# Optimization experiments

Hardware: AMD Instinct MI355X
Metric: run time of the kernel (lower is better)

The kernel has to match this reference:

```python
import jax, jax.numpy as jnp
import numpy as np

B, S, H = 2, 4096, 2048
NH, NKV, HD = 16, 4, 128          # heads, kv heads, head_dim = H // NH
GS_RATIO = 0.25                    # hardcoded in MyAttention.forward
ROPE_BASE = 10000.0


def rotate_half(x):
    h = x.shape[-1] // 2
    return jnp.concatenate((-x[..., h:], x[..., :h]), axis=-1)


def setup_inputs() -> dict:
    key = jax.random.key(0)
    ks = jax.random.split(key, 5)
    g = int(S * GS_RATIO)
    hidden_states = jax.random.normal(ks[0], (B, S, H), jnp.float32)
    position_ids = jnp.tile(jnp.arange(S, dtype=jnp.int32)[None, :], (B, 1))
    # causal additive mask per group window (0 keep, -1e9 masked)
    i = jnp.arange(g)
    causal = i[None, :] <= i[:, None]
    attention_mask = jnp.broadcast_to(
        jnp.where(causal, 0.0, -1e9).astype(jnp.float32)[None, None], (B, 1, g, g)
    )
    sc = 0.02
    Wq = (jax.random.normal(ks[1], (H, NH * HD), jnp.float32) * sc)
    Wk = (jax.random.normal(ks[2], (H, NKV * HD), jnp.float32) * sc)
    Wv = (jax.random.normal(ks[3], (H, NKV * HD), jnp.float32) * sc)
    Wo = (jax.random.normal(ks[4], (NH * HD, H), jnp.float32) * sc)
    return {"hidden_states": hidden_states, "attention_mask": attention_mask,
            "position_ids": position_ids, "Wq": Wq, "Wk": Wk, "Wv": Wv, "Wo": Wo}


def reference(hidden_states, attention_mask, position_ids, Wq, Wk, Wv, Wo):
    B_, S_, H_ = hidden_states.shape
    g = int(S_ * GS_RATIO)
    ng = S_ // g
    n_rep = NH // NKV

    # QKV projections -> (B, heads, S, HD)
    q = (hidden_states @ Wq).reshape(B_, S_, NH, HD).transpose(0, 2, 1, 3)
    k = (hidden_states @ Wk).reshape(B_, S_, NKV, HD).transpose(0, 2, 1, 3)
    v = (hidden_states @ Wv).reshape(B_, S_, NKV, HD).transpose(0, 2, 1, 3)

    # RoPE
    inv_freq = 1.0 / (ROPE_BASE ** (jnp.arange(0, HD, 2, dtype=jnp.float32) / HD))
    t = jnp.arange(S_, dtype=jnp.float32)
    emb = jnp.concatenate([jnp.outer(t, inv_freq)] * 2, axis=-1)  # (S, HD)
    cos = jnp.cos(emb)[position_ids][:, None]  # (B,1,S,HD)
    sin = jnp.sin(emb)[position_ids][:, None]
    q = q * cos + rotate_half(q) * sin
    k = k * cos + rotate_half(k) * sin

    # GQA repeat_kv
    k = jnp.repeat(k, n_rep, axis=1)
    v = jnp.repeat(v, n_rep, axis=1)

    # S2-Attn shift: roll second half of heads by -g/2 along seq, then group
    def shift(x):
        x = jnp.concatenate([x[:, :NH // 2],
                             jnp.roll(x[:, NH // 2:], -g // 2, axis=2)], axis=1)
        return x.transpose(0, 2, 1, 3).reshape(B_ * ng, g, NH, HD).transpose(0, 2, 1, 3)

    q, k, v = shift(q), shift(k), shift(v)

    attn = jnp.einsum('bhqd,bhkd->bhqk', q, k) / np.float32(np.sqrt(HD))
    mask = jnp.tile(attention_mask, (ng, 1, 1, 1))  # (B*ng,1,g,g)
    attn = attn + mask
    attn = jax.nn.softmax(attn.astype(jnp.float32), axis=-1).astype(q.dtype)

    out = jnp.einsum('bhqk,bhkd->bhqd', attn, v)  # (B*ng, NH, g, HD)
    out = out.transpose(0, 2, 1, 3).reshape(B_, S_, NH, HD)
    # undo shift for second half of heads (+g/2 along seq)
    out = jnp.concatenate([out[:, :, :NH // 2],
                           jnp.roll(out[:, :, NH // 2:], g // 2, axis=1)], axis=2)
    out = out.reshape(B_, S_, NH * HD) @ Wo
    return out
```

## Files before the change

### kernel.cpp

```cpp
#include <hip/hip_runtime.h>
#include <math.h>

typedef unsigned short u16;
typedef short bf16x8 __attribute__((ext_vector_type(8)));
typedef float f32x4 __attribute__((ext_vector_type(4)));


__device__ __forceinline__ u16 f2bf(float x) {
  union { float f; unsigned u; } c; c.f = x;
  unsigned r = (c.u + 0x7FFFu + ((c.u >> 16) & 1u)) >> 16;
  return (u16)r;
}
__device__ __forceinline__ float bf2f(u16 x) {
  union { unsigned u; float f; } c; c.u = ((unsigned)x) << 16;
  return c.f;
}

#define GLD16(gp, lp)                                                   \
  __builtin_amdgcn_global_load_lds(                                     \
      (__attribute__((address_space(1))) void*)(gp),                    \
      (__attribute__((address_space(3))) void*)(lp), 16, 0, 0)

__global__ __launch_bounds__(256) void cast_bf16_vec(
    const float* __restrict__ X, u16* __restrict__ Y) {
  const size_t i = ((size_t)blockIdx.x * 256 + threadIdx.x) * 4;
  float4 v = *(const float4*)(X + i);
  ushort4 o;
  o.x = f2bf(v.x); o.y = f2bf(v.y); o.z = f2bf(v.z); o.w = f2bf(v.w);
  *(ushort4*)(Y + i) = o;
}

__global__ __launch_bounds__(256) void wt_cast(
    const float* __restrict__ W, u16* __restrict__ Wt, int K, int N) {
  const int bk = blockIdx.y * 64;
  const int bn = blockIdx.x * 64;
  __shared__ float T[64 * 65];
  const int tid = threadIdx.x;
  #pragma unroll
  for (int u = 0; u < 16; ++u) {
    int idx = tid + u * 256;
    int kl = idx >> 6, nl = idx & 63;
    T[kl * 65 + nl] = W[(size_t)(bk + kl) * N + bn + nl];
  }
  __syncthreads();
  #pragma unroll
  for (int u = 0; u < 16; ++u) {
    int idx = tid + u * 256;
    int nl = idx >> 6, kl = idx & 63;
    Wt[(size_t)(bn + nl) * K + bk + kl] = f2bf(T[kl * 65 + nl]);
  }
}

__global__ __launch_bounds__(256) void gemm_bf16(
    const u16* __restrict__ A, const u16* __restrict__ Bt,
    float* __restrict__ Cf, u16* __restrict__ Cb, int M, int N, int K) {
  __shared__ u16 As[128 * 32];
  __shared__ u16 Bs[128 * 32];

  const int tid = threadIdx.x;
  const int bm = blockIdx.y * 128;
  const int bn = blockIdx.x * 128;
  const int w = tid >> 6, lane = tid & 63;
  const int col = lane & 15, quad = lane >> 4;
  const int mblk = (w & 1) * 64, nblk = (w >> 1) * 64;

  const int srow = tid >> 2;
  const int sseg = (tid & 3) * 8;

  const u16* ag0 = A + (size_t)(bm + srow) * K + sseg;
  const u16* ag1 = A + (size_t)(bm + 64 + srow) * K + sseg;
  const u16* bg0 = Bt + (size_t)(bn + srow) * K + sseg;
  const u16* bg1 = Bt + (size_t)(bn + 64 + srow) * K + sseg;
  u16* al = &As[srow * 32 + sseg];
  u16* bl = &Bs[srow * 32 + sseg];

  f32x4 acc[4][4];
  #pragma unroll
  for (int i = 0; i < 4; ++i)
    #pragma unroll
    for (int j = 0; j < 4; ++j) acc[i][j] = (f32x4)(0.0f);

  for (int k0 = 0; k0 < K; k0 += 32) {
    __syncthreads();
    GLD16(ag0 + k0, al);
    GLD16(ag1 + k0, al + 64 * 32);
    GLD16(bg0 + k0, bl);
    GLD16(bg1 + k0, bl + 64 * 32);
    __syncthreads();

    bf16x8 af[4], bfr[4];
    #pragma unroll
    for (int i = 0; i < 4; ++i)
      af[i] = *(const bf16x8*)&As[(mblk + 16 * i + col) * 32 + quad * 8];
    #pragma unroll
    for (int j = 0; j < 4; ++j)
      bfr[j] = *(const bf16x8*)&Bs[(nblk + 16 * j + col) * 32 + quad * 8];
    #pragma unroll
    for (int i = 0; i < 4; ++i)
      #pragma unroll
      for (int j = 0; j < 4; ++j)
        acc[i][j] = __builtin_amdgcn_mfma_f32_16x16x32_bf16(af[i], bfr[j], acc[i][j], 0, 0, 0);
  }

  #pragma unroll
  for (int i = 0; i < 4; ++i) {
    const int row0 = bm + mblk + 16 * i + quad * 4;
    #pragma unroll
    for (int j = 0; j < 4; ++j) {
      const int cc = bn + nblk + 16 * j + col;
      #pragma unroll
      for (int r = 0; r < 4; ++r) {
        if (Cb) Cb[(size_t)(row0 + r) * N + cc] = f2bf(acc[i][j][r]);
        else    Cf[(size_t)(row0 + r) * N + cc] = acc[i][j][r];
      }
    }
  }
}

__global__ __launch_bounds__(256) void rope_qkv(
    u16* __restrict__ QKV, const int* __restrict__ pos) {
  const unsigned idx = blockIdx.x * 256 + threadIdx.x;
  const int d = idx & 63;
  const unsigned rest = idx >> 6;
  const int hh = rest % 20;
  const unsigned bs = rest / 20;

  const int colbase = (hh < 16) ? hh * 128 : 2048 + (hh - 16) * 128;
  u16* p = QKV + (size_t)bs * 3072 + colbase + d;
  const float x0 = bf2f(p[0]);
  const float x1 = bf2f(p[64]);
  const float t = (float)pos[bs];
  const float inv_freq = __expf((float)d * -0.14391156509676332f);
  float s, c;
  __sincosf(t * inv_freq, &s, &c);
  const float sc = (hh < 16) ? 0.08838834764831845f : 1.0f;
  p[0]  = f2bf((x0 * c - x1 * s) * sc);
  p[64] = f2bf((x1 * c + x0 * s) * sc);
}

__global__ __launch_bounds__(256) void v_transpose(
    const u16* __restrict__ QKV, u16* __restrict__ Vt) {
  const int bid = blockIdx.x;
  const int st = bid & 63;
  const int kvh = (bid >> 6) & 3;
  const int b = bid >> 8;
  __shared__ u16 T[64 * 136];
  const int tid = threadIdx.x;
  #pragma unroll
  for (int u = 0; u < 4; ++u) {
    int idx = tid + u * 256;
    int sl = idx >> 4, ch = idx & 15;
    *(uint4*)&T[sl * 136 + ch * 8] =
        *(const uint4*)(QKV + ((size_t)(b * 4096 + st * 64 + sl)) * 3072 + 2560 + kvh * 128 + ch * 8);
  }
  __syncthreads();
  #pragma unroll
  for (int u = 0; u < 32; ++u) {
    int idx = tid + u * 256;
    int d = idx >> 6, sl = idx & 63;
    Vt[((size_t)((b * 4 + kvh) * 128 + d)) * 4096 + st * 64 + sl] = T[sl * 136 + d];
  }
}

__global__ __launch_bounds__(512, 4) void attn_mfma(
    const u16* __restrict__ QKV, const u16* __restrict__ Vt,
    u16* __restrict__ Ob) {
  __shared__ u16 Ks[64 * 136];
  __shared__ u16 Vs[128 * 72];
  __shared__ u16 Ps[8][16 * 72];

  const int bid = blockIdx.x;
  const int qt = 7 - (bid & 7);
  const int h  = (bid >> 3) & 15;
  const int gi = (bid >> 7) & 3;
  const int b  = bid >> 9;

  const int tid = threadIdx.x;
  const int w = tid >> 6, lane = tid & 63;
  const int col = lane & 15, quad = lane >> 4;

  const int shift = (h >= 8) ? 512 : 0;
  const int base_s = gi * 1024;
  const int kvh = h >> 2;
  const int ktmax = 2 * qt + 1;

  const int krow = tid >> 4, kch = tid & 15;
  const int vrow = tid >> 3, vch = tid & 7;

  const u16* ksrc = QKV + ((size_t)(b * 4096)) * 3072 + 2048 + kvh * 128;
  const u16* vsrc = Vt + ((size_t)((b * 4 + kvh) * 128)) * 4096;

  uint4 kreg[2], vreg[2];
  {
    const int sk0 = (base_s + shift) & 4095;
    kreg[0] = *(const uint4*)(ksrc + (size_t)(sk0 + krow) * 3072 + kch * 8);
    kreg[1] = *(const uint4*)(ksrc + (size_t)(sk0 + 32 + krow) * 3072 + kch * 8);
    vreg[0] = *(const uint4*)(vsrc + (size_t)vrow * 4096 + sk0 + vch * 8);
    vreg[1] = *(const uint4*)(vsrc + (size_t)(64 + vrow) * 4096 + sk0 + vch * 8);
  }

  bf16x8 aq[4];
  {
    const int qg = qt * 128 + w * 16 + col;
    const int sqr = (base_s + qg + shift) & 4095;
    const u16* qp = QKV + ((size_t)(b * 4096 + sqr)) * 3072 + h * 128;
    #pragma unroll
    for (int kk = 0; kk < 4; ++kk)
      aq[kk] = *(const bf16x8*)(qp + kk * 32 + quad * 8);
  }

  f32x4 o[8];
  #pragma unroll
  for (int jd = 0; jd < 8; ++jd) o[jd] = (f32x4)(0.0f);
  float lp[4] = {0.0f, 0.0f, 0.0f, 0.0f};

  u16* Pw = &Ps[w][0];
  const int qrow_l = qt * 128 + w * 16 + quad * 4;

  for (int kt = 0; kt <= ktmax; ++kt) {
    __syncthreads();
    *(uint4*)&Ks[krow * 136 + kch * 8] = kreg[0];
    *(uint4*)&Ks[(32 + krow) * 136 + kch * 8] = kreg[1];
    *(uint4*)&Vs[vrow * 72 + vch * 8] = vreg[0];
    *(uint4*)&Vs[(64 + vrow) * 72 + vch * 8] = vreg[1];
    __syncthreads();

    if (kt < ktmax) {
      const int skn = (base_s + (kt + 1) * 64 + shift) & 4095;
      kreg[0] = *(const uint4*)(ksrc + (size_t)(skn + krow) * 3072 + kch * 8);
      kreg[1] = *(const uint4*)(ksrc + (size_t)(skn + 32 + krow) * 3072 + kch * 8);
      vreg[0] = *(const uint4*)(vsrc + (size_t)vrow * 4096 + skn + vch * 8);
      vreg[1] = *(const uint4*)(vsrc + (size_t)(64 + vrow) * 4096 + skn + vch * 8);
    }

    f32x4 sc[4];
    #pragma unroll
    for (int j = 0; j < 4; ++j) sc[j] = (f32x4)(0.0f);
    #pragma unroll
    for (int kk = 0; kk < 4; ++kk) {
      #pragma unroll
      for (int j = 0; j < 4; ++j) {
        bf16x8 bk = *(const bf16x8*)&Ks[(16 * j + col) * 136 + kk * 32 + quad * 8];
        sc[j] = __builtin_amdgcn_mfma_f32_16x16x32_bf16(aq[kk], bk, sc[j], 0, 0, 0);
      }
    }

    if (kt >= 2 * qt) {
      #pragma unroll
      for (int j = 0; j < 4; ++j) {
        #pragma unroll
        for (int r = 0; r < 4; ++r) {
          float p = __expf(sc[j][r]);
          if ((kt * 64 + 16 * j + col) > (qrow_l + r)) p = 0.0f;
          lp[r] += p;
          Pw[(quad * 4 + r) * 72 + 16 * j + col] = f2bf(p);
        }
      }
    } else {
      #pragma unroll
      for (int j = 0; j < 4; ++j) {
        #pragma unroll
        for (int r = 0; r < 4; ++r) {
          float p = __expf(sc[j][r]);
          lp[r] += p;
          Pw[(quad * 4 + r) * 72 + 16 * j + col] = f2bf(p);
        }
      }
    }

    #pragma unroll
    for (int ks = 0; ks < 2; ++ks) {
      bf16x8 ap = *(const bf16x8*)&Pw[col * 72 + ks * 32 + quad * 8];
      #pragma unroll
      for (int jd = 0; jd < 8; ++jd) {
        bf16x8 bv = *(const bf16x8*)&Vs[(16 * jd + col) * 72 + ks * 32 + quad * 8];
        o[jd] = __builtin_amdgcn_mfma_f32_16x16x32_bf16(ap, bv, o[jd], 0, 0, 0);
      }
    }
  }

  #pragma unroll
  for (int r = 0; r < 4; ++r) {
    lp[r] += __shfl_xor(lp[r], 1, 64);
    lp[r] += __shfl_xor(lp[r], 2, 64);
    lp[r] += __shfl_xor(lp[r], 4, 64);
    lp[r] += __shfl_xor(lp[r], 8, 64);
  }

  #pragma unroll
  for (int r = 0; r < 4; ++r) {
    const int qg = qt * 128 + w * 16 + quad * 4 + r;
    const int sq = (base_s + qg + shift) & 4095;
    u16* dst = Ob + ((size_t)(b * 4096 + sq)) * 2048 + h * 128;
    const float inv = 1.0f / lp[r];
    #pragma unroll
    for (int jd = 0; jd < 8; ++jd)
      dst[16 * jd + col] = f2bf(o[jd][r] * inv);
  }
}

extern "C" void kernel_launch(void* const* d_in, const int* in_sizes, int n_in,
                              void* d_out, int out_size, void* d_ws, size_t ws_size,
                              hipStream_t stream) {
  const float* hs = (const float*)d_in[0];
  const int*   pos = (const int*)d_in[2];
  const float* Wq = (const float*)d_in[3];
  const float* Wk = (const float*)d_in[4];
  const float* Wv = (const float*)d_in[5];
  const float* Wo = (const float*)d_in[6];

  char* ws = (char*)d_ws;
  u16* hsb   = (u16*)ws; ws += (size_t)8192 * 2048 * 2;
  u16* Wqkvt = (u16*)ws; ws += (size_t)3072 * 2048 * 2;
  u16* Wot   = (u16*)ws; ws += (size_t)2048 * 2048 * 2;
  u16* QKVb  = (u16*)ws; ws += (size_t)8192 * 3072 * 2;
  u16* Vtt   = (u16*)ws; ws += (size_t)2 * 4 * 128 * 4096 * 2;
  u16* Obh   = (u16*)ws; ws += (size_t)8192 * 2048 * 2;

  dim3 blk(256);

  cast_bf16_vec<<<16384, blk, 0, stream>>>(hs, hsb);
  wt_cast<<<dim3(32, 32), blk, 0, stream>>>(Wq, Wqkvt, 2048, 2048);
  wt_cast<<<dim3(8, 32),  blk, 0, stream>>>(Wk, Wqkvt + (size_t)2048 * 2048, 2048, 512);
  wt_cast<<<dim3(8, 32),  blk, 0, stream>>>(Wv, Wqkvt + (size_t)2560 * 2048, 2048, 512);
  wt_cast<<<dim3(32, 32), blk, 0, stream>>>(Wo, Wot, 2048, 2048);

  gemm_bf16<<<dim3(24, 64), blk, 0, stream>>>(hsb, Wqkvt, nullptr, QKVb, 8192, 3072, 2048);

  rope_qkv<<<40960, blk, 0, stream>>>(QKVb, pos);
  v_transpose<<<512, blk, 0, stream>>>(QKVb, Vtt);

  attn_mfma<<<1024, dim3(512), 0, stream>>>(QKVb, Vtt, Obh);

  gemm_bf16<<<dim3(16, 64), blk, 0, stream>>>(Obh, Wot, (float*)d_out, nullptr, 8192, 2048, 2048);
}
```

Baseline: 606.6 us.

## Transpose score MFMA, vectorize P stores, drop K/V register prefetch for occupancy

Swaps the MFMA operand order so each lane holds four consecutive keys for one query, which lets P be written to LDS as packed ushort4 stores and reduces the row-sum to a single accumulator finished with two cross-lane shuffles. Removes the register double-buffered K/V prefetch and loads the current tile directly before the barrier, and raises the launch-bounds occupancy hint from 4 to 6. The aim is lower register pressure and fewer LDS store instructions, giving more resident waves per CU. In exchange, global load latency is no longer overlapped with compute inside a block and has to be hidden by the other resident waves.

```diff
diff --git a/kernel.cpp b/kernel.cpp
--- a/kernel.cpp
+++ b/kernel.cpp
@@ -162,7 +162,7 @@
   }
 }
 
-__global__ __launch_bounds__(512, 4) void attn_mfma(
+__global__ __launch_bounds__(512, 6) void attn_mfma(
     const u16* __restrict__ QKV, const u16* __restrict__ Vt,
     u16* __restrict__ Ob) {
   __shared__ u16 Ks[64 * 136];
@@ -190,15 +190,6 @@
   const u16* ksrc = QKV + ((size_t)(b * 4096)) * 3072 + 2048 + kvh * 128;
   const u16* vsrc = Vt + ((size_t)((b * 4 + kvh) * 128)) * 4096;
 
-  uint4 kreg[2], vreg[2];
-  {
-    const int sk0 = (base_s + shift) & 4095;
-    kreg[0] = *(const uint4*)(ksrc + (size_t)(sk0 + krow) * 3072 + kch * 8);
-    kreg[1] = *(const uint4*)(ksrc + (size_t)(sk0 + 32 + krow) * 3072 + kch * 8);
-    vreg[0] = *(const uint4*)(vsrc + (size_t)vrow * 4096 + sk0 + vch * 8);
-    vreg[1] = *(const uint4*)(vsrc + (size_t)(64 + vrow) * 4096 + sk0 + vch * 8);
-  }
-
   bf16x8 aq[4];
   {
     const int qg = qt * 128 + w * 16 + col;
@@ -212,59 +203,66 @@
   f32x4 o[8];
   #pragma unroll
   for (int jd = 0; jd < 8; ++jd) o[jd] = (f32x4)(0.0f);
-  float lp[4] = {0.0f, 0.0f, 0.0f, 0.0f};
+  float lsum = 0.0f;
 
   u16* Pw = &Ps[w][0];
-  const int qrow_l = qt * 128 + w * 16 + quad * 4;
+  const int qrow = qt * 128 + w * 16 + col;
 
   for (int kt = 0; kt <= ktmax; ++kt) {
+    const int sk0 = (base_s + kt * 64 + shift) & 4095;
+
+    uint4 k0 = *(const uint4*)(ksrc + (size_t)(sk0 + krow) * 3072 + kch * 8);
+    uint4 k1 = *(const uint4*)(ksrc + (size_t)(sk0 + 32 + krow) * 3072 + kch * 8);
+    uint4 v0 = *(const uint4*)(vsrc + (size_t)vrow * 4096 + sk0 + vch * 8);
+    uint4 v1 = *(const uint4*)(vsrc + (size_t)(64 + vrow) * 4096 + sk0 + vch * 8);
+
     __syncthreads();
-    *(uint4*)&Ks[krow * 136 + kch * 8] = kreg[0];
-    *(uint4*)&Ks[(32 + krow) * 136 + kch * 8] = kreg[1];
-    *(uint4*)&Vs[vrow * 72 + vch * 8] = vreg[0];
-    *(uint4*)&Vs[(64 + vrow) * 72 + vch * 8] = vreg[1];
+    *(uint4*)&Ks[krow * 136 + kch * 8] = k0;
+    *(uint4*)&Ks[(32 + krow) * 136 + kch * 8] = k1;
+    *(uint4*)&Vs[vrow * 72 + vch * 8] = v0;
+    *(uint4*)&Vs[(64 + vrow) * 72 + vch * 8] = v1;
     __syncthreads();
 
-    if (kt < ktmax) {
-      const int skn = (base_s + (kt + 1) * 64 + shift) & 4095;
-      kreg[0] = *(const uint4*)(ksrc + (size_t)(skn + krow) * 3072 + kch * 8);
-      kreg[1] = *(const uint4*)(ksrc + (size_t)(skn + 32 + krow) * 3072 + kch * 8);
-      vreg[0] = *(const uint4*)(vsrc + (size_t)vrow * 4096 + skn + vch * 8);
-      vreg[1] = *(const uint4*)(vsrc + (size_t)(64 + vrow) * 4096 + skn + vch * 8);
+    f32x4 sc[4];
+    #pragma unroll
+    for (int i = 0; i < 4; ++i) sc[i] = (f32x4)(0.0f);
+    #pragma unroll
+    for (int kk = 0; kk < 4; ++kk) {
+      #pragma unroll
+      for (int i = 0; i < 4; ++i) {
+        bf16x8 ak = *(const bf16x8*)&Ks[(16 * i + col) * 136 + kk * 32 + quad * 8];
+        sc[i] = __builtin_amdgcn_mfma_f32_16x16x32_bf16(ak, aq[kk], sc[i], 0, 0, 0);
+      }
     }
 
-    f32x4 sc[4];
-    #pragma unroll
-    for (int j = 0; j < 4; ++j) sc[j] = (f32x4)(0.0f);
-    #pragma unroll
-    for (int kk = 0; kk < 4; ++kk) {
-      #pragma unroll
-      for (int j = 0; j < 4; ++j) {
-        bf16x8 bk = *(const bf16x8*)&Ks[(16 * j + col) * 136 + kk * 32 + quad * 8];
-        sc[j] = __builtin_amdgcn_mfma_f32_16x16x32_bf16(aq[kk], bk, sc[j], 0, 0, 0);
-      }
-    }
-
-    if (kt >= 2 * qt) {
-      #pragma unroll
-      for (int j = 0; j < 4; ++j) {
-        #pragma unroll
-        for (int r = 0; r < 4; ++r) {
-          float p = __expf(sc[j][r]);
-          if ((kt * 64 + 16 * j + col) > (qrow_l + r)) p = 0.0f;
-          lp[r] += p;
-          Pw[(quad * 4 + r) * 72 + 16 * j + col] = f2bf(p);
-        }
+    if (kt * 64 + 63 > qt * 128 + w * 16) {
+      #pragma unroll
+      for (int i = 0; i < 4; ++i) {
+        ushort4 pk;
+        float p0 = __expf(sc[i][0]);
+        float p1 = __expf(sc[i][1]);
+        float p2 = __expf(sc[i][2]);
+        float p3 = __expf(sc[i][3]);
+        const int key0 = kt * 64 + 16 * i + quad * 4;
+        if (key0 + 0 > qrow) p0 = 0.0f;
+        if (key0 + 1 > qrow) p1 = 0.0f;
+        if (key0 + 2 > qrow) p2 = 0.0f;
+        if (key0 + 3 > qrow) p3 = 0.0f;
+        lsum += (p0 + p1) + (p2 + p3);
+        pk.x = f2bf(p0); pk.y = f2bf(p1); pk.z = f2bf(p2); pk.w = f2bf(p3);
+        *(ushort4*)&Pw[col * 72 + 16 * i + quad * 4] = pk;
       }
     } else {
       #pragma unroll
-      for (int j = 0; j < 4; ++j) {
-        #pragma unroll
-        for (int r = 0; r < 4; ++r) {
-          float p = __expf(sc[j][r]);
-          lp[r] += p;
-          Pw[(quad * 4 + r) * 72 + 16 * j + col] = f2bf(p);
-        }
+      for (int i = 0; i < 4; ++i) {
+        ushort4 pk;
+        float p0 = __expf(sc[i][0]);
+        float p1 = __expf(sc[i][1]);
+        float p2 = __expf(sc[i][2]);
+        float p3 = __expf(sc[i][3]);
+        lsum += (p0 + p1) + (p2 + p3);
+        pk.x = f2bf(p0); pk.y = f2bf(p1); pk.z = f2bf(p2); pk.w = f2bf(p3);
+        *(ushort4*)&Pw[col * 72 + 16 * i + quad * 4] = pk;
       }
     }
 
@@ -279,20 +277,15 @@
     }
   }
 
+  lsum += __shfl_xor(lsum, 16, 64);
+  lsum += __shfl_xor(lsum, 32, 64);
+
   #pragma unroll
   for (int r = 0; r < 4; ++r) {
-    lp[r] += __shfl_xor(lp[r], 1, 64);
-    lp[r] += __shfl_xor(lp[r], 2, 64);
-    lp[r] += __shfl_xor(lp[r], 4, 64);
-    lp[r] += __shfl_xor(lp[r], 8, 64);
-  }
-
-  #pragma unroll
-  for (int r = 0; r < 4; ++r) {
+    const float inv = 1.0f / __shfl(lsum, quad * 4 + r, 64);
     const int qg = qt * 128 + w * 16 + quad * 4 + r;
     const int sq = (base_s + qg + shift) & 4095;
     u16* dst = Ob + ((size_t)(b * 4096 + sq)) * 2048 + h * 128;
-    const float inv = 1.0f / lp[r];
     #pragma unroll
     for (int jd = 0; jd < 8; ++jd)
       dst[16 * jd + col] = f2bf(o[jd][r] * inv);
```

Measured after the change: 592.2 us. 2.4% less time.
